# Kernel optimization log

Measured on AMD Instinct MI355X. Metric: run time of the kernel, lower is better.

The kernel has to match this reference:

```python
import jax, jax.numpy as jnp
import numpy as np

B, L, D, K = 32, 128, 400, 40
RTOL, ATOL = 1e-4, 1e-6


def setup_inputs() -> dict:
    key = jax.random.key(0)
    ks = jax.random.split(key, 9)
    s = 0.3                      # input scale keeps exp(energy) in fp32 range
    u = 1.0 / np.sqrt(D)         # param scale
    input_h = jax.random.normal(ks[0], (B, L, D), jnp.float32) * s
    input_c = jax.random.normal(ks[1], (B, L, D), jnp.float32) * s
    W_d = jax.random.normal(ks[2], (K, D), jnp.float32) * u
    W_e = jax.random.normal(ks[3], (K, D), jnp.float32) * u
    U = jax.random.normal(ks[4], (K, D, D), jnp.float32) * u
    b = jax.random.normal(ks[5], (K,), jnp.float32) * 0.1
    heads = jax.random.randint(ks[6], (B, L), 0, L)
    pos = jnp.arange(L)[None, :]
    heads = jnp.where(heads == pos, (heads + 1) % L, heads)  # no self-loops (diag is -inf)
    arc_tags = jax.random.randint(ks[7], (B, L), 0, K)
    lengths = jax.random.randint(ks[8], (B,), L // 2, L + 1)
    mask = (jnp.arange(L)[None, :] < lengths[:, None]).astype(jnp.float32)
    return {"input_h": input_h, "input_c": input_c, "W_d": W_d, "W_e": W_e,
            "U": U, "b": b, "mask": mask, "heads": heads,
            "arc_tags": arc_tags, "lengths": lengths}


def reference(input_h, input_c, W_d, W_e, U, b, mask, heads, arc_tags, lengths):
    Bsz, Ln, _ = input_h.shape
    # --- BiAAttention: energy[b,k,head,child] ---
    bil = jnp.einsum('bhd,kde,bce->bkhc', input_h, U, input_c)
    sd = jnp.einsum('kd,bhd->bkh', W_d, input_h)[:, :, :, None]   # head bias
    se = jnp.einsum('kd,bcd->bkc', W_e, input_c)[:, :, None, :]   # child bias
    energy = bil + sd + se + b[None, :, None, None]
    energy = energy * mask[:, None, :, None] * mask[:, None, None, :]
    eye = jnp.eye(Ln, dtype=energy.dtype)
    energy = energy + jnp.where(eye > 0, -jnp.inf, 0.0)           # no self-arcs
    # --- Matrix-Tree partition function ---
    A = jnp.exp(energy) * mask[:, None, :, None] * mask[:, None, None, :]
    A = A.sum(axis=1)                                             # [B,L,L] over labels
    Dg = A.sum(axis=1) * (1.0 + RTOL) + ATOL                      # column (in-degree) sums
    Lap = eye * Dg[:, None, :] - A                                # Laplacian
    Sub = Lap[:, 1:, 1:]                                          # drop root row/col
    valid = jnp.arange(Ln - 1)[None, :] < (lengths - 1)[:, None]
    vm = valid[:, :, None] & valid[:, None, :]
    Sub = jnp.where(vm, Sub, jnp.eye(Ln - 1, dtype=Sub.dtype))    # identity-pad = logdet of [1:len,1:len]
    z = jnp.linalg.slogdet(Sub)[1]                                # [B]
    # --- gold-tree energy ---
    bi = jnp.arange(Bsz)[:, None]
    pos = jnp.arange(Ln)[None, :]
    te = energy[bi, arc_tags, heads, pos]                         # [B,L]
    tgt = te[:, 1:].sum(axis=1)
    return z - tgt
```

## Files before the change

kernel.cpp:

```cpp
#include <hip/hip_runtime.h>
#include <hip/hip_bf16.h>

#define BB 32
#define LL 128
#define DD 400
#define KK 40
#define EE 416
#define SDN 50
#define SEN 52

typedef __attribute__((ext_vector_type(8)))  short  bfrag;
typedef __attribute__((ext_vector_type(16))) float  ffrag;

static __device__ __forceinline__ short f2bf(float f) {
    union { float f; unsigned u; } v; v.f = f;
    unsigned r = (v.u + 0x7FFF + ((v.u >> 16) & 1)) >> 16;
    return (short)r;
}

#define MFMA32(a, b, c) __builtin_amdgcn_mfma_f32_32x32x16_bf16((a), (b), (c), 0, 0, 0)

static __device__ __forceinline__ void fzero(ffrag& f) {
#pragma unroll
    for (int r = 0; r < 16; ++r) f[r] = 0.f;
}

__global__ __launch_bounds__(256) void p_prep(
    const float* __restrict__ H, const float* __restrict__ C,
    const float* __restrict__ U,
    short* __restrict__ Hs, short* __restrict__ Cs, short* __restrict__ Us)
{
    int id = blockIdx.x * 256 + threadIdx.x;
    if (id < BB*SDN*LL) {
        int b = id / (SDN*LL); int r = id % (SDN*LL);
        int sd = r / LL; int h = r % LL;
        const float* src = H + ((size_t)(b*LL + h))*DD + sd*8;
        bfrag v;
#pragma unroll
        for (int j = 0; j < 8; ++j) v[j] = f2bf(src[j]);
        *(bfrag*)(Hs + (size_t)id*8) = v;
    } else if (id < BB*SDN*LL + BB*SEN*LL) {
        id -= BB*SDN*LL;
        int b = id / (SEN*LL); int r = id % (SEN*LL);
        int se = r / LL; int c = r % LL;
        bfrag v;
#pragma unroll
        for (int j = 0; j < 8; ++j) {
            int e = se*8 + j;
            v[j] = (e < DD) ? f2bf(C[((size_t)(b*LL + c))*DD + e]) : (short)0;
        }
        *(bfrag*)(Cs + (size_t)id*8) = v;
    } else {
        id -= BB*SDN*LL + BB*SEN*LL;
        int k = id / (SDN*EE); int r = id % (SDN*EE);
        int sd = r / EE; int e = r % EE;
        bfrag v;
#pragma unroll
        for (int j = 0; j < 8; ++j)
            v[j] = (e < DD) ? f2bf(U[((size_t)k*DD + sd*8 + j)*DD + e]) : (short)0;
        *(bfrag*)(Us + (size_t)id*8) = v;
    }
}

__global__ __launch_bounds__(256) void k_sdse(
    const float* __restrict__ H, const float* __restrict__ C,
    const float* __restrict__ Wd, const float* __restrict__ We,
    float* __restrict__ SD, float* __restrict__ SE, float* __restrict__ tgt)
{
    const int b   = blockIdx.x;
    const int rg  = blockIdx.y;
    const int srcC = blockIdx.z;
    const int t = threadIdx.x;

    if (rg == 0 && srcC == 0 && t == 0) tgt[b] = 0.f;

    __shared__ float Wl[KK*DD];
    {
        const float4* Wsrc = (const float4*)(srcC ? We : Wd);
        for (int i = t; i < KK*DD/4; i += 256) ((float4*)Wl)[i] = Wsrc[i];
    }
    __syncthreads();

    const int task = t >> 3;
    const int p    = t & 7;
    const int row  = rg*32 + task;
    const float* X = (srcC ? C : H) + ((size_t)(b*LL + row))*DD + p*50;

    float2 x[25];
#pragma unroll
    for (int i = 0; i < 25; ++i) x[i] = ((const float2*)X)[i];

    float* out = (srcC ? SE : SD) + (size_t)b*KK*LL + row;
    const float* Wb = Wl + p*50;

    for (int k = 0; k < KK; ++k) {
        const float2* wp = (const float2*)(Wb + k*DD);
        float s0 = 0.f, s1 = 0.f;
#pragma unroll
        for (int i = 0; i < 24; i += 2) {
            float2 w0 = wp[i], w1 = wp[i+1];
            s0 = fmaf(x[i].x,   w0.x, s0); s0 = fmaf(x[i].y,   w0.y, s0);
            s1 = fmaf(x[i+1].x, w1.x, s1); s1 = fmaf(x[i+1].y, w1.y, s1);
        }
        { float2 w0 = wp[24]; s0 = fmaf(x[24].x, w0.x, s0); s0 = fmaf(x[24].y, w0.y, s0); }
        float s = s0 + s1;
        s += __shfl_xor(s, 1); s += __shfl_xor(s, 2); s += __shfl_xor(s, 4);
        if (p == 0) out[k*LL] = s;
    }
}

static __device__ __forceinline__ void t_write(
    short* __restrict__ Ping, const ffrag& T, int et, int ht, int l31, int kh)
{
#pragma unroll
    for (int q = 0; q < 4; ++q) {
        const int e_base = 32*et + 8*q + 4*kh;
        if (e_base < DD) {
            const int r = 4*q;
            uint2 v;
            v.x = (unsigned)(unsigned short)f2bf(T[r])
                | ((unsigned)(unsigned short)f2bf(T[r+1]) << 16);
            v.y = (unsigned)(unsigned short)f2bf(T[r+2])
                | ((unsigned)(unsigned short)f2bf(T[r+3]) << 16);
            *(uint2*)(&Ping[((size_t)(e_base>>3)*LL + 32*ht + l31)*8 + (e_base&7)]) = v;
        }
    }
}

__global__ __launch_bounds__(1024) void k_mfma(
    const short* __restrict__ Hs, const short* __restrict__ Cs,
    const short* __restrict__ Us,
    const float* __restrict__ SD, const float* __restrict__ SE,
    const float* __restrict__ bvec, const float* __restrict__ mask,
    const int* __restrict__ heads, const int* __restrict__ tags,
    float* __restrict__ A8, float* __restrict__ tgt)
{
    const int b  = blockIdx.x;
    const int g  = blockIdx.y;
    const int t  = threadIdx.x;
    const int w  = t >> 6;
    const int l31 = t & 31;
    const int kh  = (t >> 5) & 1;

    __shared__ short Ping[SDN*LL*8];

    const size_t hsB = (size_t)b * SDN * LL;
    const size_t csB = (size_t)b * SEN * LL;

    const int ht2 = w >> 2;
    const int ct  = w & 3;
    const int hbase = 32*ht2 + 4*kh;
    const int c0 = 32*ct + l31;
    const float mc0 = mask[b*LL + c0];
    const int head0 = heads[b*LL + c0];
    const int tag0  = tags[b*LL + c0];
    unsigned vb = 0;
#pragma unroll
    for (int r = 0; r < 16; ++r) {
        const int hr = hbase + (r&3) + 8*(r>>2);
        if (mask[b*LL + hr] != 0.f && mc0 != 0.f && hr != c0) vb |= 1u << r;
    }

    ffrag E; fzero(E);

    for (int kk = 0; kk < 5; ++kk) {
        const int k = g + 8*kk;

        __syncthreads();

        {
            const uint4* src = (const uint4*)(Hs + hsB*8);
            uint4* dst = (uint4*)Ping;
            for (int i = t; i < SDN*LL*8*2/16; i += 1024) dst[i] = src[i];
        }
        __syncthreads();

        ffrag T0, T1, T2, T3;
        if (w < 13) {
            fzero(T0); fzero(T1); fzero(T2); fzero(T3);
            const int et = w;
            const short* up = Us + (((size_t)k*SDN + kh)*EE + 32*et + l31)*8;
            const short* hb = Ping + ((size_t)kh*LL + l31)*8;
#define UPF(j)    (*(const bfrag*)(up + (size_t)(j)*(2*EE*8)))
#define HPF(j,ht) (*(const bfrag*)(hb + ((size_t)(2*(j))*LL + 32*(ht))*8))
            bfrag a0 = UPF(0), a1 = UPF(1);
            bfrag hA = HPF(0,0), hB = HPF(0,1);
#pragma unroll 1
            for (int j = 0; j < 23; ++j) {
                bfrag hC = HPF(j,2), hD = HPF(j,3);
                T0 = MFMA32(a0, hA, T0);
                T1 = MFMA32(a0, hB, T1);
                bfrag hA2 = HPF(j+1,0), hB2 = HPF(j+1,1);
                bfrag an  = UPF(j+2);
                T2 = MFMA32(a0, hC, T2);
                T3 = MFMA32(a0, hD, T3);
                a0 = a1; a1 = an; hA = hA2; hB = hB2;
            }
            {
                bfrag hC = HPF(23,2), hD = HPF(23,3);
                T0 = MFMA32(a0, hA, T0);
                T1 = MFMA32(a0, hB, T1);
                bfrag hA2 = HPF(24,0), hB2 = HPF(24,1);
                T2 = MFMA32(a0, hC, T2);
                T3 = MFMA32(a0, hD, T3);
                a0 = a1; hA = hA2; hB = hB2;
            }
            {
                bfrag hC = HPF(24,2), hD = HPF(24,3);
                T0 = MFMA32(a0, hA, T0);
                T1 = MFMA32(a0, hB, T1);
                T2 = MFMA32(a0, hC, T2);
                T3 = MFMA32(a0, hD, T3);
            }
#undef UPF
#undef HPF
        }
        __syncthreads();

        if (w < 13) {
            t_write(Ping, T0, w, 0, l31, kh);
            t_write(Ping, T1, w, 1, l31, kh);
            t_write(Ping, T2, w, 2, l31, kh);
            t_write(Ping, T3, w, 3, l31, kh);
        }
        __syncthreads();

        ffrag S; fzero(S);
        const short* ta = Ping + ((size_t)kh*LL + 32*ht2 + l31)*8;
        const short* cp = Cs + (csB + (size_t)kh*LL + 32*ct + l31)*8;
#define TAF(j) (*(const bfrag*)(ta + (size_t)(2*(j))*(LL*8)))
#define CPF(j) (*(const bfrag*)(cp + (size_t)(2*(j))*(LL*8)))
        bfrag c0f = CPF(0), c1f = CPF(1), c2f = CPF(2);
        bfrag t0f = TAF(0), t1f = TAF(1);
#pragma unroll 1
        for (int j = 0; j < 22; ++j) {
            bfrag cn = CPF(j+3);
            bfrag tn = TAF(j+2);
            S = MFMA32(t0f, c0f, S);
            t0f = t1f; t1f = tn;
            c0f = c1f; c1f = c2f; c2f = cn;
        }
        S = MFMA32(t0f, c0f, S);
        S = MFMA32(t1f, c1f, S);
        S = MFMA32(TAF(24), c2f, S);
#undef TAF
#undef CPF

        const float bk = bvec[k];
        const float* SDb = SD + ((size_t)b*KK + k)*LL;
        const float sev = SE[((size_t)b*KK + k)*LL + c0];
#pragma unroll
        for (int r = 0; r < 16; ++r) {
            const int hr = hbase + (r&3) + 8*(r>>2);
            const float ev = S[r] + SDb[hr] + sev + bk;
            if ((vb >> r) & 1) {
                E[r] += __expf(ev);
                if (c0 >= 1 && tag0 == k && head0 == hr) atomicAdd(&tgt[b], ev);
            }
        }
    }

    float* Ab = A8 + ((size_t)(g*BB + b))*LL*LL;
#pragma unroll
    for (int r = 0; r < 16; ++r) {
        const int hr = hbase + (r&3) + 8*(r>>2);
        Ab[hr*LL + c0] = E[r];
    }
}

__global__ __launch_bounds__(256) void k_logdet(
    const float* __restrict__ A8, const int* __restrict__ lengths,
    const float* __restrict__ tgt, float* __restrict__ out)
{
    const int b = blockIdx.x;
    const int t = threadIdx.x;
    const int rg = t >> 4;
    const int cg = t & 15;

    __shared__ float As[LL*LL];
    __shared__ float Dg[128];
    __shared__ float Lbuf[128];
    __shared__ float Ubuf[128];
    __shared__ float red[256];

    const float4* A4 = (const float4*)A8;
    for (int f4 = t; f4 < 4096; f4 += 256) {
        float4 s = make_float4(0.f, 0.f, 0.f, 0.f);
#pragma unroll
        for (int g = 0; g < 8; ++g) {
            float4 v = A4[((size_t)(g*BB + b))*4096 + f4];
            s.x += v.x; s.y += v.y; s.z += v.z; s.w += v.w;
        }
        ((float4*)As)[f4] = s;
    }
    __syncthreads();

    {
        const int col = t & 127, half = t >> 7;
        float s = 0.f;
        for (int hr = half*64; hr < half*64 + 64; ++hr) s += As[hr*LL + col];
        red[t] = s;
    }
    __syncthreads();
    if (t < 128) Dg[t] = (red[t] + red[t+128]) * (1.0f + 1e-4f) + 1e-6f;
    __syncthreads();

    const int n1 = lengths[b] - 1;
    float m[8][8];
#pragma unroll
    for (int r = 0; r < 8; ++r) {
        const int i = 8*rg + r;
#pragma unroll
        for (int c = 0; c < 8; ++c) {
            const int j = 8*cg + c;
            float v;
            if (i < n1 && j < n1)
                v = ((i == j) ? Dg[i+1] : 0.f) - As[(i+1)*LL + (j+1)];
            else
                v = (i == j) ? 1.f : 0.f;
            m[r][c] = v;
        }
    }
    __syncthreads();

    for (int j = 0; j < 127; ++j) {
        const int jg = j >> 3, jl = j & 7;
        if (cg == jg) {
#pragma unroll
            for (int c = 0; c < 8; ++c) {
                if (c == jl) {
#pragma unroll
                    for (int r = 0; r < 8; ++r) Lbuf[8*rg + r] = m[r][c];
                }
            }
        }
        if (rg == jg) {
#pragma unroll
            for (int r = 0; r < 8; ++r) {
                if (r == jl) {
#pragma unroll
                    for (int c = 0; c < 8; ++c) Ubuf[8*cg + c] = m[r][c];
                }
            }
        }
        __syncthreads();

        const float piv = Lbuf[j];
        if (t == j) Dg[j] = piv;
        const float rp = 1.0f / piv;
        float lr[8], ur[8];
#pragma unroll
        for (int r = 0; r < 8; ++r) lr[r] = Lbuf[8*rg + r] * rp;
#pragma unroll
        for (int c = 0; c < 8; ++c) ur[c] = Ubuf[8*cg + c];
#pragma unroll
        for (int r = 0; r < 8; ++r)
#pragma unroll
            for (int c = 0; c < 8; ++c)
                m[r][c] = fmaf(-lr[r], ur[c], m[r][c]);
        __syncthreads();
    }

    float lsum = 0.f;
    if (t < 127) lsum = logf(Dg[t]);
    red[t] = lsum;
    __syncthreads();
    for (int off = 128; off >= 1; off >>= 1) {
        if (t < off) red[t] += red[t + off];
        __syncthreads();
    }
    if (t == 0) out[b] = red[0] - tgt[b];
}

extern "C" void kernel_launch(void* const* d_in, const int* in_sizes, int n_in,
                              void* d_out, int out_size, void* d_ws, size_t ws_size,
                              hipStream_t stream) {
    const float* H    = (const float*)d_in[0];
    const float* C    = (const float*)d_in[1];
    const float* Wd   = (const float*)d_in[2];
    const float* We   = (const float*)d_in[3];
    const float* U    = (const float*)d_in[4];
    const float* bv   = (const float*)d_in[5];
    const float* mask = (const float*)d_in[6];
    const int* heads  = (const int*)d_in[7];
    const int* tags   = (const int*)d_in[8];
    const int* lens   = (const int*)d_in[9];
    float* out = (float*)d_out;

    char* p = (char*)d_ws;
    float* A8  = (float*)p;                 p += (size_t)8*BB*LL*LL*4;
    float* tgt = (float*)p;                 p += 32*4;
    float* SDp = (float*)p;                 p += (size_t)BB*KK*LL*4;
    float* SEp = (float*)p;                 p += (size_t)BB*KK*LL*4;
    short* Hsp = (short*)p;                 p += (size_t)BB*SDN*LL*8*2;
    short* Csp = (short*)p;                 p += (size_t)BB*SEN*LL*8*2;
    short* Usp = (short*)p;                 p += (size_t)KK*SDN*EE*8*2;

    p_prep<<<dim3(4882), 256, 0, stream>>>(H, C, U, Hsp, Csp, Usp);
    k_sdse<<<dim3(BB, 4, 2), 256, 0, stream>>>(H, C, Wd, We, SDp, SEp, tgt);
    k_mfma<<<dim3(BB, 8), 1024, 0, stream>>>(Hsp, Csp, Usp, SDp, SEp, bv, mask,
                                             heads, tags, A8, tgt);
    k_logdet<<<dim3(BB), 256, 0, stream>>>(A8, lens, tgt, out);
}
```

Before: 337.7 us.

## Split label-sum into parallel kernel, double-buffer LU, retile MFMA waves

Moves the 8-way partial sum over label groups and the column-degree sums out of the 32-block logdet kernel into a new 512-block reduction kernel, so that work gets more parallelism. The LU loop now uses double-buffered pivot row and column buffers, which removes one barrier per step. It also stops at the sentence length instead of 127 and skips updates on tiles outside the valid region. The first MFMA stage is retiled so each wave computes a 2x2 block of fragments across 14 waves to reuse operands better, and the second-stage prefetch depth is increased. In exchange it adds a kernel launch, extra global traffic for Asum, and atomics on Dgw.

```diff
diff --git a/kernel.cpp b/kernel.cpp
--- a/kernel.cpp
+++ b/kernel.cpp
@@ -65,14 +65,18 @@
 __global__ __launch_bounds__(256) void k_sdse(
     const float* __restrict__ H, const float* __restrict__ C,
     const float* __restrict__ Wd, const float* __restrict__ We,
-    float* __restrict__ SD, float* __restrict__ SE, float* __restrict__ tgt)
+    float* __restrict__ SD, float* __restrict__ SE,
+    float* __restrict__ tgt, float* __restrict__ Dgw)
 {
     const int b   = blockIdx.x;
     const int rg  = blockIdx.y;
     const int srcC = blockIdx.z;
     const int t = threadIdx.x;
 
-    if (rg == 0 && srcC == 0 && t == 0) tgt[b] = 0.f;
+    if (srcC == 0) {
+        if (rg == 0 && t == 0) tgt[b] = 0.f;
+        if (t < 32) Dgw[b*128 + rg*32 + t] = 0.f;
+    }
 
     __shared__ float Wl[KK*DD];
     {
@@ -147,6 +151,11 @@
     const size_t hsB = (size_t)b * SDN * LL;
     const size_t csB = (size_t)b * SEN * LL;
 
+    const int ep = w >> 1;
+    const int hp = w & 1;
+    const bool p1on = (w < 14);
+    const bool has1 = (ep < 6);
+
     const int ht2 = w >> 2;
     const int ct  = w & 3;
     const int hbase = 32*ht2 + 4*kh;
@@ -175,53 +184,67 @@
         }
         __syncthreads();
 
-        ffrag T0, T1, T2, T3;
-        if (w < 13) {
-            fzero(T0); fzero(T1); fzero(T2); fzero(T3);
-            const int et = w;
-            const short* up = Us + (((size_t)k*SDN + kh)*EE + 32*et + l31)*8;
-            const short* hb = Ping + ((size_t)kh*LL + l31)*8;
-#define UPF(j)    (*(const bfrag*)(up + (size_t)(j)*(2*EE*8)))
-#define HPF(j,ht) (*(const bfrag*)(hb + ((size_t)(2*(j))*LL + 32*(ht))*8))
-            bfrag a0 = UPF(0), a1 = UPF(1);
-            bfrag hA = HPF(0,0), hB = HPF(0,1);
+        ffrag T00, T01, T10, T11;
+        if (p1on) {
+            fzero(T00); fzero(T01); fzero(T10); fzero(T11);
+            const short* up0 = Us + (((size_t)k*SDN + kh)*EE + 32*(2*ep) + l31)*8;
+            const short* hb  = Ping + ((size_t)kh*LL + 64*hp + l31)*8;
+#define U0F(j) (*(const bfrag*)(up0 + (size_t)(j)*(2*EE*8)))
+#define U1F(j) (*(const bfrag*)(up0 + 32*8 + (size_t)(j)*(2*EE*8)))
+#define H0F(j) (*(const bfrag*)(hb + (size_t)(2*(j))*(LL*8)))
+#define H1F(j) (*(const bfrag*)(hb + 32*8 + (size_t)(2*(j))*(LL*8)))
+            bfrag a0A = U0F(0), a0B = U0F(1);
+            bfrag a1A = a0A, a1B = a0B;
+            if (has1) { a1A = U1F(0); a1B = U1F(1); }
+            bfrag h0 = H0F(0), h1 = H1F(0);
 #pragma unroll 1
             for (int j = 0; j < 23; ++j) {
-                bfrag hC = HPF(j,2), hD = HPF(j,3);
-                T0 = MFMA32(a0, hA, T0);
-                T1 = MFMA32(a0, hB, T1);
-                bfrag hA2 = HPF(j+1,0), hB2 = HPF(j+1,1);
-                bfrag an  = UPF(j+2);
-                T2 = MFMA32(a0, hC, T2);
-                T3 = MFMA32(a0, hD, T3);
-                a0 = a1; a1 = an; hA = hA2; hB = hB2;
+                bfrag h0n = H0F(j+1), h1n = H1F(j+1);
+                bfrag a0n = U0F(j+2);
+                T00 = MFMA32(a0A, h0, T00);
+                T01 = MFMA32(a0A, h1, T01);
+                if (has1) {
+                    bfrag a1n = U1F(j+2);
+                    T10 = MFMA32(a1A, h0, T10);
+                    T11 = MFMA32(a1A, h1, T11);
+                    a1A = a1B; a1B = a1n;
+                }
+                a0A = a0B; a0B = a0n;
+                h0 = h0n; h1 = h1n;
             }
             {
-                bfrag hC = HPF(23,2), hD = HPF(23,3);
-                T0 = MFMA32(a0, hA, T0);
-                T1 = MFMA32(a0, hB, T1);
-                bfrag hA2 = HPF(24,0), hB2 = HPF(24,1);
-                T2 = MFMA32(a0, hC, T2);
-                T3 = MFMA32(a0, hD, T3);
-                a0 = a1; hA = hA2; hB = hB2;
+                bfrag h0n = H0F(24), h1n = H1F(24);
+                T00 = MFMA32(a0A, h0, T00);
+                T01 = MFMA32(a0A, h1, T01);
+                if (has1) {
+                    T10 = MFMA32(a1A, h0, T10);
+                    T11 = MFMA32(a1A, h1, T11);
+                    a1A = a1B;
+                }
+                a0A = a0B; h0 = h0n; h1 = h1n;
             }
             {
-                bfrag hC = HPF(24,2), hD = HPF(24,3);
-                T0 = MFMA32(a0, hA, T0);
-                T1 = MFMA32(a0, hB, T1);
-                T2 = MFMA32(a0, hC, T2);
-                T3 = MFMA32(a0, hD, T3);
-            }
-#undef UPF
-#undef HPF
-        }
-        __syncthreads();
-
-        if (w < 13) {
-            t_write(Ping, T0, w, 0, l31, kh);
-            t_write(Ping, T1, w, 1, l31, kh);
-            t_write(Ping, T2, w, 2, l31, kh);
-            t_write(Ping, T3, w, 3, l31, kh);
+                T00 = MFMA32(a0A, h0, T00);
+                T01 = MFMA32(a0A, h1, T01);
+                if (has1) {
+                    T10 = MFMA32(a1A, h0, T10);
+                    T11 = MFMA32(a1A, h1, T11);
+                }
+            }
+#undef U0F
+#undef U1F
+#undef H0F
+#undef H1F
+        }
+        __syncthreads();
+
+        if (p1on) {
+            t_write(Ping, T00, 2*ep,   2*hp,   l31, kh);
+            t_write(Ping, T01, 2*ep,   2*hp+1, l31, kh);
+            if (has1) {
+                t_write(Ping, T10, 2*ep+1, 2*hp,   l31, kh);
+                t_write(Ping, T11, 2*ep+1, 2*hp+1, l31, kh);
+            }
         }
         __syncthreads();
 
@@ -230,19 +253,25 @@
         const short* cp = Cs + (csB + (size_t)kh*LL + 32*ct + l31)*8;
 #define TAF(j) (*(const bfrag*)(ta + (size_t)(2*(j))*(LL*8)))
 #define CPF(j) (*(const bfrag*)(cp + (size_t)(2*(j))*(LL*8)))
-        bfrag c0f = CPF(0), c1f = CPF(1), c2f = CPF(2);
-        bfrag t0f = TAF(0), t1f = TAF(1);
+        bfrag c0f=CPF(0), c1f=CPF(1), c2f=CPF(2), c3f=CPF(3), c4f=CPF(4), c5f=CPF(5);
+        bfrag t0f=TAF(0), t1f=TAF(1), t2f=TAF(2);
 #pragma unroll 1
-        for (int j = 0; j < 22; ++j) {
-            bfrag cn = CPF(j+3);
-            bfrag tn = TAF(j+2);
+        for (int j = 0; j < 19; ++j) {
+            bfrag cn = CPF(j+6), tn = TAF(j+3);
             S = MFMA32(t0f, c0f, S);
-            t0f = t1f; t1f = tn;
-            c0f = c1f; c1f = c2f; c2f = cn;
-        }
+            t0f=t1f; t1f=t2f; t2f=tn;
+            c0f=c1f; c1f=c2f; c2f=c3f; c3f=c4f; c4f=c5f; c5f=cn;
+        }
+#pragma unroll 1
+        for (int j = 19; j < 22; ++j) {
+            bfrag tn = TAF(j+3);
+            S = MFMA32(t0f, c0f, S);
+            t0f=t1f; t1f=t2f; t2f=tn;
+            c0f=c1f; c1f=c2f; c2f=c3f; c3f=c4f;
+        }
+        S = MFMA32(t0f, c0f, S); t0f=t1f; c0f=c1f; t1f=t2f; c1f=c2f;
+        S = MFMA32(t0f, c0f, S); t0f=t1f; c0f=c1f;
         S = MFMA32(t0f, c0f, S);
-        S = MFMA32(t1f, c1f, S);
-        S = MFMA32(TAF(24), c2f, S);
 #undef TAF
 #undef CPF
 
@@ -268,8 +297,38 @@
     }
 }
 
+__global__ __launch_bounds__(256) void k_sum(
+    const float* __restrict__ A8, float* __restrict__ Asum,
+    float* __restrict__ Dgw)
+{
+    const int b = blockIdx.x >> 4;
+    const int seg = blockIdx.x & 15;
+    const int t = threadIdx.x;
+    __shared__ float cs[128];
+    if (t < 128) cs[t] = 0.f;
+    __syncthreads();
+
+    const int f4 = seg*256 + t;
+    float4 s = make_float4(0.f, 0.f, 0.f, 0.f);
+#pragma unroll
+    for (int g = 0; g < 8; ++g) {
+        float4 v = ((const float4*)A8)[((size_t)(g*BB + b))*4096 + f4];
+        s.x += v.x; s.y += v.y; s.z += v.z; s.w += v.w;
+    }
+    ((float4*)Asum)[(size_t)b*4096 + f4] = s;
+
+    const int c4 = (f4 & 31) * 4;
+    atomicAdd(&cs[c4+0], s.x);
+    atomicAdd(&cs[c4+1], s.y);
+    atomicAdd(&cs[c4+2], s.z);
+    atomicAdd(&cs[c4+3], s.w);
+    __syncthreads();
+    if (t < 128) atomicAdd(&Dgw[b*128 + t], cs[t]);
+}
+
 __global__ __launch_bounds__(256) void k_logdet(
-    const float* __restrict__ A8, const int* __restrict__ lengths,
+    const float* __restrict__ Asum, const float* __restrict__ Dgw,
+    const int* __restrict__ lengths,
     const float* __restrict__ tgt, float* __restrict__ out)
 {
     const int b = blockIdx.x;
@@ -278,31 +337,16 @@
     const int cg = t & 15;
 
     __shared__ float As[LL*LL];
-    __shared__ float Dg[128];
-    __shared__ float Lbuf[128];
-    __shared__ float Ubuf[128];
+    __shared__ float DgS[128];
+    __shared__ float Lb[2][128];
+    __shared__ float Ub[2][128];
     __shared__ float red[256];
 
-    const float4* A4 = (const float4*)A8;
-    for (int f4 = t; f4 < 4096; f4 += 256) {
-        float4 s = make_float4(0.f, 0.f, 0.f, 0.f);
-#pragma unroll
-        for (int g = 0; g < 8; ++g) {
-            float4 v = A4[((size_t)(g*BB + b))*4096 + f4];
-            s.x += v.x; s.y += v.y; s.z += v.z; s.w += v.w;
-        }
-        ((float4*)As)[f4] = s;
-    }
-    __syncthreads();
-
     {
-        const int col = t & 127, half = t >> 7;
-        float s = 0.f;
-        for (int hr = half*64; hr < half*64 + 64; ++hr) s += As[hr*LL + col];
-        red[t] = s;
-    }
-    __syncthreads();
-    if (t < 128) Dg[t] = (red[t] + red[t+128]) * (1.0f + 1e-4f) + 1e-6f;
+        const float4* A4 = (const float4*)(Asum + (size_t)b*LL*LL);
+        for (int i = t; i < 4096; i += 256) ((float4*)As)[i] = A4[i];
+    }
+    if (t < 128) DgS[t] = Dgw[b*128 + t] * (1.0f + 1e-4f) + 1e-6f;
     __syncthreads();
 
     const int n1 = lengths[b] - 1;
@@ -315,7 +359,7 @@
             const int j = 8*cg + c;
             float v;
             if (i < n1 && j < n1)
-                v = ((i == j) ? Dg[i+1] : 0.f) - As[(i+1)*LL + (j+1)];
+                v = ((i == j) ? DgS[i+1] : 0.f) - As[(i+1)*LL + (j+1)];
             else
                 v = (i == j) ? 1.f : 0.f;
             m[r][c] = v;
@@ -323,14 +367,15 @@
     }
     __syncthreads();
 
-    for (int j = 0; j < 127; ++j) {
-        const int jg = j >> 3, jl = j & 7;
+    const bool act = (8*rg < n1) && (8*cg < n1);
+    for (int j = 0; j < n1; ++j) {
+        const int bu = j & 1, jg = j >> 3, jl = j & 7;
         if (cg == jg) {
 #pragma unroll
             for (int c = 0; c < 8; ++c) {
                 if (c == jl) {
 #pragma unroll
-                    for (int r = 0; r < 8; ++r) Lbuf[8*rg + r] = m[r][c];
+                    for (int r = 0; r < 8; ++r) Lb[bu][8*rg + r] = m[r][c];
                 }
             }
         }
@@ -339,30 +384,32 @@
             for (int r = 0; r < 8; ++r) {
                 if (r == jl) {
 #pragma unroll
-                    for (int c = 0; c < 8; ++c) Ubuf[8*cg + c] = m[r][c];
+                    for (int c = 0; c < 8; ++c) Ub[bu][8*cg + c] = m[r][c];
                 }
             }
         }
         __syncthreads();
 
-        const float piv = Lbuf[j];
-        if (t == j) Dg[j] = piv;
-        const float rp = 1.0f / piv;
-        float lr[8], ur[8];
-#pragma unroll
-        for (int r = 0; r < 8; ++r) lr[r] = Lbuf[8*rg + r] * rp;
-#pragma unroll
-        for (int c = 0; c < 8; ++c) ur[c] = Ubuf[8*cg + c];
-#pragma unroll
-        for (int r = 0; r < 8; ++r)
-#pragma unroll
-            for (int c = 0; c < 8; ++c)
-                m[r][c] = fmaf(-lr[r], ur[c], m[r][c]);
-        __syncthreads();
-    }
+        const float piv = Lb[bu][j];
+        if (t == j) DgS[j] = piv;
+        if (act) {
+            const float rp = 1.0f / piv;
+            float lr[8], ur[8];
+#pragma unroll
+            for (int r = 0; r < 8; ++r) lr[r] = Lb[bu][8*rg + r] * rp;
+#pragma unroll
+            for (int c = 0; c < 8; ++c) ur[c] = Ub[bu][8*cg + c];
+#pragma unroll
+            for (int r = 0; r < 8; ++r)
+#pragma unroll
+                for (int c = 0; c < 8; ++c)
+                    m[r][c] = fmaf(-lr[r], ur[c], m[r][c]);
+        }
+    }
+    __syncthreads();
 
     float lsum = 0.f;
-    if (t < 127) lsum = logf(Dg[t]);
+    if (t < n1) lsum = logf(DgS[t]);
     red[t] = lsum;
     __syncthreads();
     for (int off = 128; off >= 1; off >>= 1) {
@@ -388,17 +435,20 @@
     float* out = (float*)d_out;
 
     char* p = (char*)d_ws;
-    float* A8  = (float*)p;                 p += (size_t)8*BB*LL*LL*4;
-    float* tgt = (float*)p;                 p += 32*4;
-    float* SDp = (float*)p;                 p += (size_t)BB*KK*LL*4;
-    float* SEp = (float*)p;                 p += (size_t)BB*KK*LL*4;
-    short* Hsp = (short*)p;                 p += (size_t)BB*SDN*LL*8*2;
-    short* Csp = (short*)p;                 p += (size_t)BB*SEN*LL*8*2;
-    short* Usp = (short*)p;                 p += (size_t)KK*SDN*EE*8*2;
+    float* A8   = (float*)p;                p += (size_t)8*BB*LL*LL*4;
+    float* Asum = (float*)p;                p += (size_t)BB*LL*LL*4;
+    float* Dgw  = (float*)p;                p += (size_t)BB*128*4;
+    float* tgt  = (float*)p;                p += 32*4;
+    float* SDp  = (float*)p;                p += (size_t)BB*KK*LL*4;
+    float* SEp  = (float*)p;                p += (size_t)BB*KK*LL*4;
+    short* Hsp  = (short*)p;                p += (size_t)BB*SDN*LL*8*2;
+    short* Csp  = (short*)p;                p += (size_t)BB*SEN*LL*8*2;
+    short* Usp  = (short*)p;                p += (size_t)KK*SDN*EE*8*2;
 
     p_prep<<<dim3(4882), 256, 0, stream>>>(H, C, U, Hsp, Csp, Usp);
-    k_sdse<<<dim3(BB, 4, 2), 256, 0, stream>>>(H, C, Wd, We, SDp, SEp, tgt);
+    k_sdse<<<dim3(BB, 4, 2), 256, 0, stream>>>(H, C, Wd, We, SDp, SEp, tgt, Dgw);
     k_mfma<<<dim3(BB, 8), 1024, 0, stream>>>(Hsp, Csp, Usp, SDp, SEp, bv, mask,
                                              heads, tags, A8, tgt);
-    k_logdet<<<dim3(BB), 256, 0, stream>>>(A8, lens, tgt, out);
-}
+    k_sum<<<dim3(BB*16), 256, 0, stream>>>(A8, Asum, Dgw);
+    k_logdet<<<dim3(BB), 256, 0, stream>>>(Asum, Dgw, lens, tgt, out);
+}
```

After: 702.9 us. 2.08x slower.
